# Kernel tuning notes

Hardware: AMD Instinct MI355X
Metric: run time of the kernel (lower is better)

## Reference

```python
import jax, jax.numpy as jnp
import numpy as np

EPS = 1e-15
FEAT = 128
HALF = FEAT // 2
N_RBF = 20
CUTOFF = 5.0
NUM_CONV = 3
N_ATOMS = 10000
N_EDGES = 160000
N_Z = 100


def setup_inputs() -> dict:
    key = jax.random.key(0)
    ks = iter(jax.random.split(key, 40))

    def W(shape):
        fan_in = shape[-2] if len(shape) > 1 else 1
        return (jax.random.normal(next(ks), shape, jnp.float32) / np.sqrt(fan_in)).astype(jnp.float32)

    # graph
    xyz = jax.random.normal(next(ks), (N_ATOMS, 3), jnp.float32)
    z = jax.random.randint(next(ks), (N_ATOMS,), 0, N_Z)
    src = jax.random.randint(next(ks), (N_EDGES,), 0, N_ATOMS)
    off = jax.random.randint(next(ks), (N_EDGES,), 1, N_ATOMS)
    nbr_list = jnp.stack([src, (src + off) % N_ATOMS], axis=1)  # directed, no self-loops

    L = NUM_CONV
    inp = dict(
        xyz=xyz, z=z, nbr_list=nbr_list,
        embed=W((N_Z, FEAT)),
        msg_w1=W((L, FEAT, FEAT)), msg_b1=jnp.zeros((L, FEAT), jnp.float32),
        msg_w2=W((L, FEAT, 3 * FEAT)), msg_b2=jnp.zeros((L, 3 * FEAT), jnp.float32),
        dist_w=W((L, N_RBF, 3 * FEAT)), dist_b=jnp.zeros((L, 3 * FEAT), jnp.float32),
        upd_u=W((L, FEAT, FEAT)), upd_v=W((L, FEAT, FEAT)),
        upd_w1=W((L, 2 * FEAT, FEAT)), upd_b1=jnp.zeros((L, FEAT), jnp.float32),
        upd_w2=W((L, FEAT, 3 * FEAT)), upd_b2=jnp.zeros((L, 3 * FEAT), jnp.float32),
        ero_w1=W((FEAT, HALF)), ero_b1=jnp.zeros((HALF,), jnp.float32),
        ero_w2=W((HALF, 1)), ero_b2=jnp.zeros((1,), jnp.float32),
    )
    return inp


def _painn_forces(xyz, z, nbr_list, embed,
                  msg_w1, msg_b1, msg_w2, msg_b2, dist_w, dist_b,
                  upd_u, upd_v, upd_w1, upd_b1, upd_w2, upd_b2,
                  ero_w1, ero_b1, ero_w2, ero_b2):
    N = z.shape[0]
    i, j = nbr_list[:, 0], nbr_list[:, 1]
    r_ij = xyz[j] - xyz[i]                               # [E,3]
    dist = jnp.sqrt(jnp.sum(r_ij * r_ij + EPS, axis=-1))  # [E]
    unit = r_ij / dist[:, None]
    # radial basis: sin(n*pi*d/cutoff)/d, cosine cutoff envelope
    k_n = jnp.arange(1, N_RBF + 1, dtype=jnp.float32) * (np.pi / CUTOFF)
    rbf = jnp.sin(k_n * dist[:, None]) / dist[:, None]   # [E,n_rbf]
    env = jnp.where(dist < CUTOFF,
                    0.5 * (jnp.cos(np.pi * dist / CUTOFF) + 1.0), 0.0)  # [E]

    s = embed[z]                                         # [N,F]
    v = jnp.zeros((N, FEAT, 3), s.dtype)                 # [N,F,3]

    for l in range(NUM_CONV):
        # --- message block ---
        w_s = (rbf @ dist_w[l] + dist_b[l]) * env[:, None]                 # [E,3F]
        phi = jax.nn.silu(s @ msg_w1[l] + msg_b1[l]) @ msg_w2[l] + msg_b2[l]  # [N,3F]
        inv = (phi[j] * w_s).reshape(-1, 3, FEAT)                           # [E,3,F]
        dv_ij = inv[:, 0, :][..., None] * v[j] + inv[:, 2, :][..., None] * unit[:, None, :]
        ds_ij = inv[:, 1, :]
        s = s + jax.ops.segment_sum(ds_ij, i, num_segments=N)
        v = v + jax.ops.segment_sum(dv_ij, i, num_segments=N)
        # --- update block ---
        u_v = jnp.einsum('nfc,fg->ngc', v, upd_u[l])                        # [N,F,3]
        v_v = jnp.einsum('nfc,fg->ngc', v, upd_v[l])
        v_v_norm = jnp.sqrt(jnp.sum(v_v * v_v, axis=-1) + EPS)              # [N,F]
        s_stack = jnp.concatenate([s, v_v_norm], axis=-1)                   # [N,2F]
        sp = (jax.nn.silu(s_stack @ upd_w1[l] + upd_b1[l]) @ upd_w2[l] + upd_b2[l]).reshape(-1, 3, FEAT)
        v = v + u_v * sp[:, 0, :][..., None]
        s = s + jnp.sum(u_v * v_v, axis=-1) * sp[:, 1, :] + sp[:, 2, :]

    # --- edge readout -> per-atom forces ---
    e = s[i] + s[j]                                                         # [E,F]
    f_scalar = jax.nn.silu(e @ ero_w1 + ero_b1) @ ero_w2 + ero_b2           # [E,1]
    dis_vec = xyz[i] - xyz[j]
    dis = jnp.sqrt(jnp.sum(dis_vec * dis_vec, axis=1))[:, None]
    f_edge = f_scalar * (dis_vec / dis)                                     # [E,3]
    f_atom = (jax.ops.segment_sum(f_edge, i, num_segments=N)
              - jax.ops.segment_sum(f_edge, j, num_segments=N))             # [N,3]
    return f_atom


def reference(xyz, z, nbr_list, embed,
              msg_w1, msg_b1, msg_w2, msg_b2, dist_w, dist_b,
              upd_u, upd_v, upd_w1, upd_b1, upd_w2, upd_b2,
              ero_w1, ero_b1, ero_w2, ero_b2):
    return _painn_forces(xyz, z, nbr_list, embed,
                         msg_w1, msg_b1, msg_w2, msg_b2, dist_w, dist_b,
                         upd_u, upd_v, upd_w1, upd_b1, upd_w2, upd_b2,
                         ero_w1, ero_b1, ero_w2, ero_b2)
```

## Files before the change

### kernel.cpp

```cpp
#include <hip/hip_runtime.h>
#include <math.h>

#define EPS_F 1e-15f
#define NRBF 20
#define CUTOFF_F 5.0f
#define PI_F 3.14159265358979323846f

typedef unsigned short u16;
typedef _Float16 f16;
typedef f16 f16x8 __attribute__((ext_vector_type(8)));
typedef f16 f16x4 __attribute__((ext_vector_type(4)));
typedef f16 f16x2 __attribute__((ext_vector_type(2)));
typedef float floatx4 __attribute__((ext_vector_type(4)));

__device__ __forceinline__ float silu_f(float x) { return x / (1.0f + expf(-x)); }

__global__ __launch_bounds__(256) void hist_kernel(
    const int* __restrict__ nbr, int* __restrict__ hist, int E)
{
  int e = blockIdx.x * 256 + threadIdx.x;
  if (e >= E) return;
  atomicAdd(hist + nbr[2 * e], 1);
}

__global__ __launch_bounds__(1024) void scan_kernel(
    const int* __restrict__ hist, int* __restrict__ start,
    int* __restrict__ cursor, int N)
{
  __shared__ int wsum[16];
  __shared__ int carry_s;
  int tid = threadIdx.x;
  int lane = tid & 63, wid = tid >> 6;
  if (tid == 0) carry_s = 0;
  __syncthreads();
  for (int base = 0; base < N; base += 1024) {
    int x = (base + tid < N) ? hist[base + tid] : 0;
    int v = x;
#pragma unroll
    for (int o = 1; o < 64; o <<= 1) {
      int t2 = __shfl_up(v, o, 64);
      if (lane >= o) v += t2;
    }
    if (lane == 63) wsum[wid] = v;
    __syncthreads();
    if (tid < 16) {
      int w = wsum[tid];
#pragma unroll
      for (int o = 1; o < 16; o <<= 1) {
        int t2 = __shfl_up(w, o, 64);
        if (tid >= o) w += t2;
      }
      wsum[tid] = w;
    }
    __syncthreads();
    int wbase = (wid == 0) ? 0 : wsum[wid - 1];
    int incl = v + wbase;
    int carry = carry_s;
    if (base + tid < N) {
      int ex = carry + incl - x;
      start[base + tid] = ex;
      cursor[base + tid] = ex;
    }
    __syncthreads();
    if (tid == 1023) carry_s = carry + incl;
    __syncthreads();
  }
  if (tid == 0) start[N] = carry_s;
}

__global__ __launch_bounds__(256) void scatter_id_kernel(
    const int* __restrict__ nbr, int* __restrict__ cursor,
    int* __restrict__ order, int E)
{
  int e = blockIdx.x * 256 + threadIdx.x;
  if (e >= E) return;
  int pos = atomicAdd(cursor + nbr[2 * e], 1);
  order[pos] = e;
}

__global__ __launch_bounds__(256) void segsort_kernel(
    int* __restrict__ order, const int* __restrict__ start, int N)
{
  int wi = blockIdx.x * 4 + (threadIdx.x >> 6);
  int lane = threadIdx.x & 63;
  if (wi >= N) return;
  int s0 = start[wi], s1 = start[wi + 1];
  int len = s1 - s0;
  if (len <= 1) return;
  if (len <= 64) {
    int id = (lane < len) ? order[s0 + lane] : 0x7FFFFFFF;
    int rank = 0;
#pragma unroll
    for (int k = 0; k < 64; ++k) {
      int other = __shfl(id, k, 64);
      rank += (other < id) ? 1 : 0;
    }
    if (lane < len) order[s0 + rank] = id;
  } else if (lane == 0) {
    for (int a = s0 + 1; a < s1; ++a) {
      int key = order[a];
      int b = a - 1;
      while (b >= s0 && order[b] > key) { order[b + 1] = order[b]; --b; }
      order[b + 1] = key;
    }
  }
}

__global__ __launch_bounds__(256) void geom_fill_kernel(
    const int* __restrict__ order, const int* __restrict__ nbr,
    const float* __restrict__ xyz, int2* __restrict__ ij_s,
    float* __restrict__ unit_s, f16* __restrict__ rbf_h, int E)
{
  int p = blockIdx.x * 256 + threadIdx.x;
  if (p >= E) return;
  int e = order[p];
  int i = nbr[2 * e], j = nbr[2 * e + 1];
  float dx = xyz[3 * j + 0] - xyz[3 * i + 0];
  float dy = xyz[3 * j + 1] - xyz[3 * i + 1];
  float dz = xyz[3 * j + 2] - xyz[3 * i + 2];
  float d2 = dx * dx + dy * dy + dz * dz + 3.0f * EPS_F;
  float d = sqrtf(d2);
  float inv_d = 1.0f / d;
  ij_s[p] = make_int2(i, j);
  unit_s[3 * p + 0] = dx * inv_d;
  unit_s[3 * p + 1] = dy * inv_d;
  unit_s[3 * p + 2] = dz * inv_d;
  float x = d * (PI_F / CUTOFF_F);
  float s1, c1;
  __sincosf(x, &s1, &c1);
  float envv = (d < CUTOFF_F) ? 0.5f * (c1 + 1.0f) : 0.0f;
  f16 tmp[32];
  float two_c = 2.0f * c1;
  float env_inv_d = envv * inv_d;
  float sp = 0.0f, sn = s1;
  tmp[0] = (f16)(sn * env_inv_d);
#pragma unroll
  for (int n = 1; n < NRBF; ++n) {
    float nx = two_c * sn - sp;
    sp = sn; sn = nx;
    tmp[n] = (f16)(sn * env_inv_d);
  }
  tmp[NRBF] = (f16)envv;
#pragma unroll
  for (int n = NRBF + 1; n < 32; ++n) tmp[n] = (f16)0.0f;
#pragma unroll
  for (int g = 0; g < 4; ++g)
    *(f16x8*)(rbf_h + (size_t)p * 32 + g * 8) = *(f16x8*)&tmp[g * 8];
}

__global__ __launch_bounds__(256) void dwfrag_kernel(
    const float* __restrict__ dw, const float* __restrict__ db,
    f16* __restrict__ dwf)
{
  int idx = blockIdx.x * 256 + threadIdx.x;
  if (idx >= 3 * 24 * 64 * 8) return;
  int q = idx & 7;
  int lane = (idx >> 3) & 63;
  int ct = (idx >> 9) % 24;
  int l = idx / (24 * 64 * 8);
  int k = (lane >> 4) * 8 + q;
  int col = ct * 16 + (lane & 15);
  float val = 0.f;
  if (k < NRBF) val = dw[(size_t)l * NRBF * 384 + (size_t)k * 384 + col];
  else if (k == NRBF) val = db[(size_t)l * 384 + col];
  dwf[idx] = (f16)val;
}

__global__ __launch_bounds__(256) void embed_kernel(
    const int* __restrict__ z, const float* __restrict__ embed,
    float* __restrict__ s, f16* __restrict__ s_h, int N)
{
  int idx = blockIdx.x * 256 + threadIdx.x;
  if (idx >= N * 128) return;
  int n = idx >> 7, f = idx & 127;
  float x = embed[z[n] * 128 + f];
  s[idx] = x;
  s_h[idx] = (f16)x;
}

__global__ __launch_bounds__(256) void w1t_kernel(
    const float* __restrict__ w1, f16* __restrict__ w1t)
{
  int idx = blockIdx.x * 256 + threadIdx.x;
  if (idx >= 64 * 128) return;
  int n = idx >> 7, k = idx & 127;
  w1t[idx] = (f16)w1[(size_t)k * 64 + n];
}

template <bool SILU, int OUT, bool AH>
__global__ __launch_bounds__(256) void gemm_kernel(
    const void* __restrict__ Ap, const float* __restrict__ W,
    const float* __restrict__ bias, const float* __restrict__ rowscale,
    void* __restrict__ Cout, int M, int N, int K)
{
  __shared__ f16 As[64][40];
  __shared__ f16 Bs[64][40];
  int t = threadIdx.x;
  int wave = t >> 6, lane = t & 63;
  int rw = wave & 1, cw = wave >> 1;
  int lr = lane & 15, quad = lane >> 4;
  int row0 = blockIdx.x * 64, col0 = blockIdx.y * 64;
  floatx4 acc[2][2] = {};
  for (int k0 = 0; k0 < K; k0 += 32) {
    if (AH) {
      const f16* A = (const f16*)Ap;
      int sm = t >> 2, sk = (t & 3) * 8;
      f16x8 av;
      if (row0 + sm < M) av = *(const f16x8*)(A + (size_t)(row0 + sm) * K + k0 + sk);
      else { for (int q = 0; q < 8; ++q) av[q] = (f16)0.0f; }
      *(f16x8*)&As[sm][sk] = av;
    } else {
      const float* A = (const float*)Ap;
#pragma unroll
      for (int u0 = 0; u0 < 2; ++u0) {
        int u = t + u0 * 256;
        int m = u >> 3, c4 = (u & 7) * 4;
        float4 av = make_float4(0.f, 0.f, 0.f, 0.f);
        if (row0 + m < M) av = *(const float4*)(A + (size_t)(row0 + m) * K + k0 + c4);
        f16x4 hv;
        hv[0] = (f16)av.x; hv[1] = (f16)av.y; hv[2] = (f16)av.z; hv[3] = (f16)av.w;
        *(f16x4*)&As[m][c4] = hv;
      }
    }
#pragma unroll
    for (int u0 = 0; u0 < 2; ++u0) {
      int u = t + u0 * 256;
      int k = u >> 4, n4 = (u & 15) * 4;
      float4 wv = *(const float4*)(W + (size_t)(k0 + k) * N + col0 + n4);
      Bs[n4 + 0][k] = (f16)wv.x;
      Bs[n4 + 1][k] = (f16)wv.y;
      Bs[n4 + 2][k] = (f16)wv.z;
      Bs[n4 + 3][k] = (f16)wv.w;
    }
    __syncthreads();
    f16x8 af[2], bfr[2];
#pragma unroll
    for (int tr = 0; tr < 2; ++tr)
      af[tr] = *(const f16x8*)&As[rw * 32 + tr * 16 + lr][quad * 8];
#pragma unroll
    for (int tc = 0; tc < 2; ++tc)
      bfr[tc] = *(const f16x8*)&Bs[cw * 32 + tc * 16 + lr][quad * 8];
#pragma unroll
    for (int tr = 0; tr < 2; ++tr)
#pragma unroll
      for (int tc = 0; tc < 2; ++tc)
        acc[tr][tc] = __builtin_amdgcn_mfma_f32_16x16x32_f16(af[tr], bfr[tc], acc[tr][tc], 0, 0, 0);
    __syncthreads();
  }
#pragma unroll
  for (int tc = 0; tc < 2; ++tc) {
    int col = col0 + cw * 32 + tc * 16 + lr;
    float bb = bias ? bias[col] : 0.0f;
#pragma unroll
    for (int tr = 0; tr < 2; ++tr) {
#pragma unroll
      for (int r = 0; r < 4; ++r) {
        int row = row0 + rw * 32 + tr * 16 + quad * 4 + r;
        if (row < M) {
          float x = acc[tr][tc][r] + bb;
          if (rowscale) x *= rowscale[row];
          if (SILU) x = silu_f(x);
          size_t o = (size_t)row * N + col;
          if (OUT == 0) ((float*)Cout)[o] = x;
          else          ((f16*)Cout)[o] = (f16)x;
        }
      }
    }
  }
}

__global__ __launch_bounds__(256) void gemm_dual_kernel(
    const float* __restrict__ A, const float* __restrict__ W1,
    const float* __restrict__ W2, float* __restrict__ C1, float* __restrict__ C2,
    int M, int N, int K)
{
  __shared__ f16 As[64][40];
  __shared__ f16 Bs1[64][40];
  __shared__ f16 Bs2[64][40];
  int t = threadIdx.x;
  int wave = t >> 6, lane = t & 63;
  int rw = wave & 1, cw = wave >> 1;
  int lr = lane & 15, quad = lane >> 4;
  int row0 = blockIdx.x * 64, col0 = blockIdx.y * 64;
  floatx4 acc1[2][2] = {};
  floatx4 acc2[2][2] = {};
  for (int k0 = 0; k0 < K; k0 += 32) {
#pragma unroll
    for (int u0 = 0; u0 < 2; ++u0) {
      int u = t + u0 * 256;
      int m = u >> 3, c4 = (u & 7) * 4;
      float4 av = make_float4(0.f, 0.f, 0.f, 0.f);
      if (row0 + m < M) av = *(const float4*)(A + (size_t)(row0 + m) * K + k0 + c4);
      f16x4 hv;
      hv[0] = (f16)av.x; hv[1] = (f16)av.y; hv[2] = (f16)av.z; hv[3] = (f16)av.w;
      *(f16x4*)&As[m][c4] = hv;
    }
#pragma unroll
    for (int u0 = 0; u0 < 2; ++u0) {
      int u = t + u0 * 256;
      int k = u >> 4, n4 = (u & 15) * 4;
      float4 wv = *(const float4*)(W1 + (size_t)(k0 + k) * N + col0 + n4);
      Bs1[n4 + 0][k] = (f16)wv.x;
      Bs1[n4 + 1][k] = (f16)wv.y;
      Bs1[n4 + 2][k] = (f16)wv.z;
      Bs1[n4 + 3][k] = (f16)wv.w;
      float4 xv = *(const float4*)(W2 + (size_t)(k0 + k) * N + col0 + n4);
      Bs2[n4 + 0][k] = (f16)xv.x;
      Bs2[n4 + 1][k] = (f16)xv.y;
      Bs2[n4 + 2][k] = (f16)xv.z;
      Bs2[n4 + 3][k] = (f16)xv.w;
    }
    __syncthreads();
    f16x8 af[2], b1[2], b2[2];
#pragma unroll
    for (int tr = 0; tr < 2; ++tr)
      af[tr] = *(const f16x8*)&As[rw * 32 + tr * 16 + lr][quad * 8];
#pragma unroll
    for (int tc = 0; tc < 2; ++tc) {
      b1[tc] = *(const f16x8*)&Bs1[cw * 32 + tc * 16 + lr][quad * 8];
      b2[tc] = *(const f16x8*)&Bs2[cw * 32 + tc * 16 + lr][quad * 8];
    }
#pragma unroll
    for (int tr = 0; tr < 2; ++tr)
#pragma unroll
      for (int tc = 0; tc < 2; ++tc) {
        acc1[tr][tc] = __builtin_amdgcn_mfma_f32_16x16x32_f16(af[tr], b1[tc], acc1[tr][tc], 0, 0, 0);
        acc2[tr][tc] = __builtin_amdgcn_mfma_f32_16x16x32_f16(af[tr], b2[tc], acc2[tr][tc], 0, 0, 0);
      }
    __syncthreads();
  }
#pragma unroll
  for (int tc = 0; tc < 2; ++tc) {
    int col = col0 + cw * 32 + tc * 16 + lr;
#pragma unroll
    for (int tr = 0; tr < 2; ++tr) {
#pragma unroll
      for (int r = 0; r < 4; ++r) {
        int row = row0 + rw * 32 + tr * 16 + quad * 4 + r;
        if (row < M) {
          C1[(size_t)row * N + col] = acc1[tr][tc][r];
          C2[(size_t)row * N + col] = acc2[tr][tc][r];
        }
      }
    }
  }
}

#define MEPB 32
__global__ __launch_bounds__(384, 2) void message_kernel(
    const int2* __restrict__ ij_s, const float* __restrict__ unit_s,
    const f16* __restrict__ rbf_h, const f16* __restrict__ dwf,
    const f16* __restrict__ phi_h, const f16* __restrict__ vh,
    float* __restrict__ s, float* __restrict__ v, int E)
{
  __shared__ f16 rbfA[MEPB][40];
  __shared__ f16 wsT[384][38];
  __shared__ int2 ijL[MEPB];
  __shared__ float unitL[MEPB * 3];
  int t = threadIdx.x;
  int wave = t >> 6, lane = t & 63;
  int e_lo = blockIdx.x * MEPB;
  if (e_lo >= E) return;
  int e_hi = (e_lo + MEPB < E) ? e_lo + MEPB : E;
  int cnt = e_hi - e_lo;

  f16x8 bf[4];
#pragma unroll
  for (int i = 0; i < 4; ++i) {
    int ct = wave * 4 + i;
    bf[i] = *(const f16x8*)(dwf + ((size_t)ct * 64 + lane) * 8);
  }
  if (t < MEPB * 4) {
    int r = t >> 2, c8 = (t & 3) * 8;
    f16x8 rv;
    if (e_lo + r < E) rv = *(const f16x8*)(rbf_h + (size_t)(e_lo + r) * 32 + c8);
    else { for (int q = 0; q < 8; ++q) rv[q] = (f16)0.0f; }
    *(f16x8*)&rbfA[r][c8] = rv;
  }
  if (t < cnt) ijL[t] = ij_s[e_lo + t];
  if (t < cnt * 3) unitL[t] = unit_s[(size_t)e_lo * 3 + t];
  __syncthreads();

  int lr = lane & 15, quad = lane >> 4;
  f16x8 af[2];
#pragma unroll
  for (int tr = 0; tr < 2; ++tr)
    af[tr] = *(const f16x8*)&rbfA[tr * 16 + lr][quad * 8];
  floatx4 acc[2][4] = {};
#pragma unroll
  for (int tr = 0; tr < 2; ++tr)
#pragma unroll
    for (int i = 0; i < 4; ++i)
      acc[tr][i] = __builtin_amdgcn_mfma_f32_16x16x32_f16(af[tr], bf[i], acc[tr][i], 0, 0, 0);
#pragma unroll
  for (int tr = 0; tr < 2; ++tr)
#pragma unroll
    for (int i = 0; i < 4; ++i) {
      int col = (wave * 4 + i) * 16 + lr;
      int er = tr * 16 + quad * 4;
      f16x2 lo2, hi2;
      lo2[0] = (f16)acc[tr][i][0]; lo2[1] = (f16)acc[tr][i][1];
      hi2[0] = (f16)acc[tr][i][2]; hi2[1] = (f16)acc[tr][i][3];
      *(f16x2*)&wsT[col][er]     = lo2;
      *(f16x2*)&wsT[col][er + 2] = hi2;
    }
  __syncthreads();

  int g = t >> 7, f = t & 127;
  float a0 = 0.f, a1 = 0.f, a2 = 0.f;
  int prev_i = -1;
  int2 ij_c = ijL[0];
  f16 ph_c = phi_h[(size_t)ij_c.y * 384 + t];
  f16 vj0c = (f16)0.f, vj1c = (f16)0.f, vj2c = (f16)0.f;
  if (g == 0) {
    const f16* vp = vh + (size_t)ij_c.y * 384 + f;
    vj0c = vp[0]; vj1c = vp[128]; vj2c = vp[256];
  }
  for (int r = 0; r < cnt; ++r) {
    int rn = (r + 1 < cnt) ? r + 1 : r;
    int2 ij_n = ijL[rn];
    f16 ph_n = phi_h[(size_t)ij_n.y * 384 + t];
    f16 vj0n = (f16)0.f, vj1n = (f16)0.f, vj2n = (f16)0.f;
    if (g == 0) {
      const f16* vp = vh + (size_t)ij_n.y * 384 + f;
      vj0n = vp[0]; vj1n = vp[128]; vj2n = vp[256];
    }
    if (ij_c.x != prev_i) {
      if (prev_i >= 0) {
        if (g == 1) {
          atomicAdd(s + (size_t)prev_i * 128 + f, a0);
        } else {
          float* vb = v + (size_t)prev_i * 384 + f;
          atomicAdd(vb, a0);
          atomicAdd(vb + 128, a1);
          atomicAdd(vb + 256, a2);
        }
        a0 = a1 = a2 = 0.f;
      }
      prev_i = ij_c.x;
    }
    float ws = (float)wsT[t][r];
    float inv = (float)ph_c * ws;
    if (g == 0) {
      a0 = fmaf(inv, (float)vj0c, a0);
      a1 = fmaf(inv, (float)vj1c, a1);
      a2 = fmaf(inv, (float)vj2c, a2);
    } else if (g == 1) {
      a0 += inv;
    } else {
      a0 = fmaf(inv, unitL[3 * r + 0], a0);
      a1 = fmaf(inv, unitL[3 * r + 1], a1);
      a2 = fmaf(inv, unitL[3 * r + 2], a2);
    }
    ij_c = ij_n; ph_c = ph_n;
    vj0c = vj0n; vj1c = vj1n; vj2c = vj2n;
  }
  if (prev_i >= 0) {
    if (g == 1) {
      atomicAdd(s + (size_t)prev_i * 128 + f, a0);
    } else {
      float* vb = v + (size_t)prev_i * 384 + f;
      atomicAdd(vb, a0);
      atomicAdd(vb + 128, a1);
      atomicAdd(vb + 256, a2);
    }
  }
}

__global__ __launch_bounds__(256) void stack_kernel(
    const float* __restrict__ s, const float* __restrict__ v_v,
    f16* __restrict__ s_stack, int N)
{
  int idx = blockIdx.x * 256 + threadIdx.x;
  if (idx >= N * 128) return;
  int n = idx >> 7, g = idx & 127;
  float a = v_v[(size_t)n * 384 + g];
  float b = v_v[(size_t)n * 384 + 128 + g];
  float c = v_v[(size_t)n * 384 + 256 + g];
  s_stack[(size_t)n * 256 + g] = (f16)s[idx];
  s_stack[(size_t)n * 256 + 128 + g] = (f16)sqrtf(a * a + b * b + c * c + EPS_F);
}

__global__ __launch_bounds__(256) void apply_kernel(
    float* __restrict__ s, f16* __restrict__ s_h,
    float* __restrict__ v, f16* __restrict__ v_h,
    const float* __restrict__ u_v, const float* __restrict__ v_v,
    const float* __restrict__ sp, int N)
{
  int idx = blockIdx.x * 256 + threadIdx.x;
  if (idx >= N * 128) return;
  int n = idx >> 7, g = idx & 127;
  float sp0 = sp[(size_t)n * 384 + g];
  float sp1 = sp[(size_t)n * 384 + 128 + g];
  float sp2 = sp[(size_t)n * 384 + 256 + g];
  float dot = 0.f;
#pragma unroll
  for (int c = 0; c < 3; ++c) {
    size_t o = (size_t)n * 384 + c * 128 + g;
    float uv = u_v[o];
    float vn = fmaf(uv, sp0, v[o]);
    v[o] = vn;
    v_h[o] = (f16)vn;
    dot = fmaf(uv, v_v[o], dot);
  }
  float sn = s[idx] + dot * sp1 + sp2;
  s[idx] = sn;
  s_h[idx] = (f16)sn;
}

__global__ __launch_bounds__(256) void readout_gemm_kernel(
    const int* __restrict__ nbr, const float* __restrict__ xyz,
    const f16* __restrict__ s_h, const f16* __restrict__ w1t,
    const float* __restrict__ b1, const float* __restrict__ w2,
    const float* __restrict__ b2, float* __restrict__ out, int E)
{
  __shared__ f16 As[64][40];
  __shared__ f16 Bs[64][40];
  __shared__ float red[2][64];
  __shared__ int ijc[64][2];
  int t = threadIdx.x;
  int wave = t >> 6, lane = t & 63;
  int rw = wave & 1, cw = wave >> 1;
  int lr = lane & 15, quad = lane >> 4;
  int e0b = blockIdx.x * 64;
  if (t < 64) {
    int e = e0b + t;
    if (e < E) { ijc[t][0] = nbr[2 * e]; ijc[t][1] = nbr[2 * e + 1]; }
    else { ijc[t][0] = 0; ijc[t][1] = 0; }
  }
  __syncthreads();
  int m = t >> 2;
  int c8 = (t & 3) * 8;
  int im = ijc[m][0], jm = ijc[m][1];
  bool okm = (e0b + m) < E;
  f16x8 xa[4], ya[4];
  if (okm) {
#pragma unroll
    for (int w = 0; w < 4; ++w) {
      xa[w] = *(const f16x8*)(s_h + (size_t)im * 128 + w * 32 + c8);
      ya[w] = *(const f16x8*)(s_h + (size_t)jm * 128 + w * 32 + c8);
    }
  } else {
#pragma unroll
    for (int w = 0; w < 4; ++w)
      for (int q = 0; q < 8; ++q) { xa[w][q] = (f16)0.0f; ya[w][q] = (f16)0.0f; }
  }
  floatx4 acc[2][2] = {};
#pragma unroll
  for (int w = 0; w < 4; ++w) {
    *(f16x8*)&As[m][c8] = xa[w] + ya[w];
    {
      int sm = t >> 2, sk = (t & 3) * 8;
      *(f16x8*)&Bs[sm][sk] = *(const f16x8*)(w1t + (size_t)sm * 128 + w * 32 + sk);
    }
    __syncthreads();
    f16x8 af[2], bfr[2];
#pragma unroll
    for (int tr = 0; tr < 2; ++tr)
      af[tr] = *(const f16x8*)&As[rw * 32 + tr * 16 + lr][quad * 8];
#pragma unroll
    for (int tc = 0; tc < 2; ++tc)
      bfr[tc] = *(const f16x8*)&Bs[cw * 32 + tc * 16 + lr][quad * 8];
#pragma unroll
    for (int tr = 0; tr < 2; ++tr)
#pragma unroll
      for (int tc = 0; tc < 2; ++tc)
        acc[tr][tc] = __builtin_amdgcn_mfma_f32_16x16x32_f16(af[tr], bfr[tc], acc[tr][tc], 0, 0, 0);
    __syncthreads();
  }
  float b1v[2], w2v[2];
#pragma unroll
  for (int tc = 0; tc < 2; ++tc) {
    int col = cw * 32 + tc * 16 + lr;
    b1v[tc] = b1[col];
    w2v[tc] = w2[col];
  }
#pragma unroll
  for (int tr = 0; tr < 2; ++tr) {
#pragma unroll
    for (int r = 0; r < 4; ++r) {
      float p = 0.f;
#pragma unroll
      for (int tc = 0; tc < 2; ++tc)
        p += silu_f(acc[tr][tc][r] + b1v[tc]) * w2v[tc];
#pragma unroll
      for (int ofs = 1; ofs < 16; ofs <<= 1) p += __shfl_xor(p, ofs, 64);
      if (lr == 0) red[cw][rw * 32 + tr * 16 + quad * 4 + r] = p;
    }
  }
  __syncthreads();
  if (t < 64) {
    int e = e0b + t;
    if (e < E) {
      float fs = red[0][t] + red[1][t] + b2[0];
      int i = ijc[t][0], j = ijc[t][1];
      float dx = xyz[3 * i + 0] - xyz[3 * j + 0];
      float dy = xyz[3 * i + 1] - xyz[3 * j + 1];
      float dz = xyz[3 * i + 2] - xyz[3 * j + 2];
      float dis = sqrtf(dx * dx + dy * dy + dz * dz);
      float sc = fs / dis;
      float fx = sc * dx, fy = sc * dy, fz = sc * dz;
      atomicAdd(out + (size_t)i * 3 + 0, fx);
      atomicAdd(out + (size_t)i * 3 + 1, fy);
      atomicAdd(out + (size_t)i * 3 + 2, fz);
      atomicAdd(out + (size_t)j * 3 + 0, -fx);
      atomicAdd(out + (size_t)j * 3 + 1, -fy);
      atomicAdd(out + (size_t)j * 3 + 2, -fz);
    }
  }
}

extern "C" void kernel_launch(void* const* d_in, const int* in_sizes, int n_in,
                              void* d_out, int out_size, void* d_ws, size_t ws_size,
                              hipStream_t stream) {
  const float* xyz    = (const float*)d_in[0];
  const int*   z      = (const int*)d_in[1];
  const int*   nbr    = (const int*)d_in[2];
  const float* embed  = (const float*)d_in[3];
  const float* msg_w1 = (const float*)d_in[4];
  const float* msg_b1 = (const float*)d_in[5];
  const float* msg_w2 = (const float*)d_in[6];
  const float* msg_b2 = (const float*)d_in[7];
  const float* dist_w = (const float*)d_in[8];
  const float* dist_b = (const float*)d_in[9];
  const float* upd_u  = (const float*)d_in[10];
  const float* upd_v  = (const float*)d_in[11];
  const float* upd_w1 = (const float*)d_in[12];
  const float* upd_b1 = (const float*)d_in[13];
  const float* upd_w2 = (const float*)d_in[14];
  const float* upd_b2 = (const float*)d_in[15];
  const float* ero_w1 = (const float*)d_in[16];
  const float* ero_b1 = (const float*)d_in[17];
  const float* ero_w2 = (const float*)d_in[18];
  const float* ero_b2 = (const float*)d_in[19];

  const int N = in_sizes[1];
  const int E = in_sizes[2] / 2;
  const int L = 3;

  char* ws = (char*)d_ws;
  size_t off = 0;
  auto alloc = [&](size_t bytes) -> void* {
    void* p = ws + off;
    off += (bytes + 255) & ~(size_t)255;
    return p;
  };
  float* unit_s = (float*)alloc((size_t)E * 3 * 4);
  f16*   rbf_h  = (f16*)alloc((size_t)E * 32 * 2);
  int2*  ij_s   = (int2*)alloc((size_t)E * 8);
  int*   order  = (int*)alloc((size_t)E * 4);
  float* s      = (float*)alloc((size_t)N * 128 * 4);
  f16*   s_h    = (f16*)alloc((size_t)N * 128 * 2);
  float* vA     = (float*)alloc((size_t)N * 384 * 4);
  f16*   vhA    = (f16*)alloc((size_t)N * 384 * 2);
  f16*   phi_h  = (f16*)alloc((size_t)N * 384 * 2);
  f16*   w1t    = (f16*)alloc((size_t)64 * 128 * 2);
  f16*   dwf    = (f16*)alloc((size_t)3 * 24 * 64 * 8 * 2);
  int*   histx  = (int*)alloc((size_t)(N + 1) * 4);
  int*   startp = (int*)alloc((size_t)(N + 1) * 4);
  int*   cursor = (int*)alloc((size_t)N * 4);
  float* u_v    = (float*)alloc((size_t)N * 384 * 4);
  float* v_v    = (float*)alloc((size_t)N * 384 * 4);
  float* sp     = (float*)alloc((size_t)N * 384 * 4);
  f16*   sstk_h = (f16*)alloc((size_t)N * 256 * 2);
  f16*   h_h    = (f16*)alloc((size_t)N * 128 * 2);

  auto cdiv = [](int a, int b) { return (a + b - 1) / b; };

  hipMemsetAsync(vA, 0, (size_t)N * 384 * 4, stream);
  hipMemsetAsync(vhA, 0, (size_t)N * 384 * 2, stream);
  hipMemsetAsync(histx, 0, (size_t)(N + 1) * 4, stream);
  hist_kernel<<<cdiv(E, 256), 256, 0, stream>>>(nbr, histx, E);
  scan_kernel<<<1, 1024, 0, stream>>>(histx, startp, cursor, N);
  scatter_id_kernel<<<cdiv(E, 256), 256, 0, stream>>>(nbr, cursor, order, E);
  segsort_kernel<<<cdiv(N, 4), 256, 0, stream>>>(order, startp, N);
  geom_fill_kernel<<<cdiv(E, 256), 256, 0, stream>>>(
      order, nbr, xyz, ij_s, unit_s, rbf_h, E);
  embed_kernel<<<cdiv(N * 128, 256), 256, 0, stream>>>(z, embed, s, s_h, N);
  w1t_kernel<<<cdiv(64 * 128, 256), 256, 0, stream>>>(ero_w1, w1t);
  dwfrag_kernel<<<cdiv(3 * 24 * 64 * 8, 256), 256, 0, stream>>>(dist_w, dist_b, dwf);

  for (int l = 0; l < L; ++l) {
    gemm_kernel<true, 1, true><<<dim3(cdiv(N, 64), 2), 256, 0, stream>>>(
        s_h, msg_w1 + (size_t)l * 128 * 128, msg_b1 + (size_t)l * 128, nullptr, h_h, N, 128, 128);
    gemm_kernel<false, 1, true><<<dim3(cdiv(N, 64), 6), 256, 0, stream>>>(
        h_h, msg_w2 + (size_t)l * 128 * 384, msg_b2 + (size_t)l * 384, nullptr, phi_h, N, 384, 128);
    message_kernel<<<cdiv(E, MEPB), 384, 0, stream>>>(
        ij_s, unit_s, rbf_h, dwf + (size_t)l * 24 * 64 * 8,
        phi_h, vhA, s, vA, E);
    gemm_dual_kernel<<<dim3(cdiv(N * 3, 64), 2), 256, 0, stream>>>(
        vA, upd_u + (size_t)l * 128 * 128, upd_v + (size_t)l * 128 * 128,
        u_v, v_v, N * 3, 128, 128);
    stack_kernel<<<cdiv(N * 128, 256), 256, 0, stream>>>(s, v_v, sstk_h, N);
    gemm_kernel<true, 1, true><<<dim3(cdiv(N, 64), 2), 256, 0, stream>>>(
        sstk_h, upd_w1 + (size_t)l * 256 * 128, upd_b1 + (size_t)l * 128, nullptr, h_h, N, 128, 256);
    gemm_kernel<false, 0, true><<<dim3(cdiv(N, 64), 6), 256, 0, stream>>>(
        h_h, upd_w2 + (size_t)l * 128 * 384, upd_b2 + (size_t)l * 384, nullptr, sp, N, 384, 128);
    apply_kernel<<<cdiv(N * 128, 256), 256, 0, stream>>>(
        s, s_h, vA, vhA, u_v, v_v, sp, N);
  }

  hipMemsetAsync(d_out, 0, (size_t)out_size * 4, stream);
  readout_gemm_kernel<<<cdiv(E, 64), 256, 0, stream>>>(
      nbr, xyz, s_h, w1t, ero_b1, ero_w2, ero_b2, (float*)d_out, E);
}
```

Before: 768.7 us.

## Batch gather of neighbor phi and v into shared memory before message accumulation

The message kernel now gathers all phi rows and neighbor v values for the block's 32 edges into shared memory in one unrolled pass, instead of a one-deep software prefetch inside the serial accumulation loop. The goal is to expose many independent global loads at once so gather latency overlaps. The filter weights move to registers (wsr) so the wsT buffer can be reused for phi. Occupancy hint raised from 2 to 4 blocks per CU. Risks: higher register pressure from the 32-entry arrays against the tighter launch bound, and packing i/j into 16 bits each, which works for 10000 atoms but would break above 65535.

Measured after the change: 1.732 ms. 2.25x slower.

```diff
diff --git a/kernel.cpp b/kernel.cpp
--- a/kernel.cpp
+++ b/kernel.cpp
@@ -347,7 +347,7 @@
 }
 
 #define MEPB 32
-__global__ __launch_bounds__(384, 2) void message_kernel(
+__global__ __launch_bounds__(384, 4) void message_kernel(
     const int2* __restrict__ ij_s, const float* __restrict__ unit_s,
     const f16* __restrict__ rbf_h, const f16* __restrict__ dwf,
     const f16* __restrict__ phi_h, const f16* __restrict__ vh,
@@ -355,6 +355,7 @@
 {
   __shared__ f16 rbfA[MEPB][40];
   __shared__ f16 wsT[384][38];
+  __shared__ f16 vjL[3][128][34];
   __shared__ int2 ijL[MEPB];
   __shared__ float unitL[MEPB * 3];
   int t = threadIdx.x;
@@ -407,53 +408,64 @@
   __syncthreads();
 
   int g = t >> 7, f = t & 127;
+  int pij[MEPB];
+#pragma unroll
+  for (int e = 0; e < MEPB; ++e) {
+    int ee = (e < cnt) ? e : (cnt - 1);
+    pij[e] = (ijL[ee].x << 16) | (ijL[ee].y & 0xFFFF);
+  }
+  f16 wsr[MEPB];
+#pragma unroll
+  for (int e = 0; e < MEPB; ++e) wsr[e] = wsT[t][e];
+
+#pragma unroll
+  for (int e = 0; e < MEPB; ++e) {
+    if (e < cnt) {
+      int j = pij[e] & 0xFFFF;
+      wsT[t][e] = phi_h[(size_t)j * 384 + t];
+      if (g == 0) {
+        const f16* vp = vh + (size_t)j * 384 + f;
+        vjL[0][f][e] = vp[0];
+        vjL[1][f][e] = vp[128];
+        vjL[2][f][e] = vp[256];
+      }
+    }
+  }
+  __syncthreads();
+
   float a0 = 0.f, a1 = 0.f, a2 = 0.f;
   int prev_i = -1;
-  int2 ij_c = ijL[0];
-  f16 ph_c = phi_h[(size_t)ij_c.y * 384 + t];
-  f16 vj0c = (f16)0.f, vj1c = (f16)0.f, vj2c = (f16)0.f;
-  if (g == 0) {
-    const f16* vp = vh + (size_t)ij_c.y * 384 + f;
-    vj0c = vp[0]; vj1c = vp[128]; vj2c = vp[256];
-  }
-  for (int r = 0; r < cnt; ++r) {
-    int rn = (r + 1 < cnt) ? r + 1 : r;
-    int2 ij_n = ijL[rn];
-    f16 ph_n = phi_h[(size_t)ij_n.y * 384 + t];
-    f16 vj0n = (f16)0.f, vj1n = (f16)0.f, vj2n = (f16)0.f;
-    if (g == 0) {
-      const f16* vp = vh + (size_t)ij_n.y * 384 + f;
-      vj0n = vp[0]; vj1n = vp[128]; vj2n = vp[256];
-    }
-    if (ij_c.x != prev_i) {
-      if (prev_i >= 0) {
-        if (g == 1) {
-          atomicAdd(s + (size_t)prev_i * 128 + f, a0);
-        } else {
-          float* vb = v + (size_t)prev_i * 384 + f;
-          atomicAdd(vb, a0);
-          atomicAdd(vb + 128, a1);
-          atomicAdd(vb + 256, a2);
+#pragma unroll
+  for (int e = 0; e < MEPB; ++e) {
+    if (e < cnt) {
+      int i = pij[e] >> 16;
+      if (i != prev_i) {
+        if (prev_i >= 0) {
+          if (g == 1) {
+            atomicAdd(s + (size_t)prev_i * 128 + f, a0);
+          } else {
+            float* vb = v + (size_t)prev_i * 384 + f;
+            atomicAdd(vb, a0);
+            atomicAdd(vb + 128, a1);
+            atomicAdd(vb + 256, a2);
+          }
+          a0 = a1 = a2 = 0.f;
         }
-        a0 = a1 = a2 = 0.f;
+        prev_i = i;
       }
-      prev_i = ij_c.x;
-    }
-    float ws = (float)wsT[t][r];
-    float inv = (float)ph_c * ws;
-    if (g == 0) {
-      a0 = fmaf(inv, (float)vj0c, a0);
-      a1 = fmaf(inv, (float)vj1c, a1);
-      a2 = fmaf(inv, (float)vj2c, a2);
-    } else if (g == 1) {
-      a0 += inv;
-    } else {
-      a0 = fmaf(inv, unitL[3 * r + 0], a0);
-      a1 = fmaf(inv, unitL[3 * r + 1], a1);
-      a2 = fmaf(inv, unitL[3 * r + 2], a2);
-    }
-    ij_c = ij_n; ph_c = ph_n;
-    vj0c = vj0n; vj1c = vj1n; vj2c = vj2n;
+      float inv = (float)wsT[t][e] * (float)wsr[e];
+      if (g == 0) {
+        a0 = fmaf(inv, (float)vjL[0][f][e], a0);
+        a1 = fmaf(inv, (float)vjL[1][f][e], a1);
+        a2 = fmaf(inv, (float)vjL[2][f][e], a2);
+      } else if (g == 1) {
+        a0 += inv;
+      } else {
+        a0 = fmaf(inv, unitL[3 * e + 0], a0);
+        a1 = fmaf(inv, unitL[3 * e + 1], a1);
+        a2 = fmaf(inv, unitL[3 * e + 2], a2);
+      }
+    }
   }
   if (prev_i >= 0) {
     if (g == 1) {
```
